# Performance work log

Measured on AMD Instinct MI355X. Metric: run time of the kernel, lower is better.

## Reference

```python
import jax, jax.numpy as jnp
import numpy as np

N_NODES = 100000
N_EDGES = 1600000
IN_CH, HID_CH, OUT_CH = 128, 128, 64


def glorot(key, fan_in, fan_out):
    lim = np.sqrt(6.0 / (fan_in + fan_out)).astype(np.float32)
    return jax.random.uniform(key, (fan_in, fan_out), jnp.float32, -lim, lim)


def gcn_conv(x, src, dst, W, b):
    """PyG GCNConv: add self-loops, symmetric deg^-1/2 normalization,
    linear transform, scatter-add aggregation at targets, plus bias."""
    n = x.shape[0]
    xw = x @ W  # [N, F_out]
    loop = jnp.arange(n)
    s = jnp.concatenate([src, loop])  # sources (message origin)
    d = jnp.concatenate([dst, loop])  # targets (aggregation site)
    deg = jax.ops.segment_sum(jnp.ones_like(d, dtype=xw.dtype), d, num_segments=n)
    dinv = jnp.where(deg > 0, jax.lax.rsqrt(deg), 0.0)
    norm = dinv[s] * dinv[d]  # [E+N]
    out = jax.ops.segment_sum(norm[:, None] * xw[s], d, num_segments=n)
    return out + b


def setup_inputs() -> dict:
    key = jax.random.key(0)
    ks = jax.random.split(key, 8)
    x = jax.random.normal(ks[0], (N_NODES, IN_CH), jnp.float32)
    edge_index = jax.random.randint(ks[1], (2, N_EDGES), 0, N_NODES, jnp.int64)
    return {
        "x": x,
        "edge_index": edge_index,
        "W1": glorot(ks[2], IN_CH, HID_CH),
        "b1": jnp.zeros((HID_CH,), jnp.float32),
        "W2": glorot(ks[3], HID_CH, HID_CH),
        "b2": jnp.zeros((HID_CH,), jnp.float32),
        "W3": glorot(ks[4], HID_CH, OUT_CH),
        "b3": jnp.zeros((OUT_CH,), jnp.float32),
    }


def reference(x, edge_index, W1, b1, W2, b2, W3, b3):
    src, dst = edge_index[0], edge_index[1]
    # eval mode: dropout is identity
    h = jax.nn.relu(gcn_conv(x, src, dst, W1, b1))
    h = jax.nn.relu(gcn_conv(h, src, dst, W2, b2))
    h = gcn_conv(h, src, dst, W3, b3)
    return jax.nn.log_softmax(h, axis=1)
```

## Files before the change

kernel.cpp:

```cpp
#include <hip/hip_runtime.h>
#include <math.h>


#define NN 100000
#define NE 1600000
#define NBUK 391
#define BCAP 4608

typedef float floatx4 __attribute__((ext_vector_type(4)));
typedef short short8 __attribute__((ext_vector_type(8)));

__device__ __forceinline__ unsigned short f2bf(float f) {
    unsigned u = __float_as_uint(f);
    unsigned r = (u + 0x7fffu + ((u >> 16) & 1u)) >> 16;
    return (unsigned short)r;
}
__device__ __forceinline__ float bflo(unsigned u) { return __uint_as_float(u << 16); }
__device__ __forceinline__ float bfhi(unsigned u) { return __uint_as_float(u & 0xffff0000u); }

__global__ __launch_bounds__(256) void k_wprep(const float* __restrict__ W, unsigned short* __restrict__ Wtg,
                                               int K, int NC) {
    int idx = blockIdx.x * 256 + threadIdx.x;
    if (idx >= NC * K) return;
    int n = idx / K, k = idx - n * K;
    Wtg[idx] = f2bf(W[k * NC + n]);
}

__global__ __launch_bounds__(256) void k_bucket(const int4* __restrict__ src4, const int4* __restrict__ dst4,
                                                int* __restrict__ bcur, int* __restrict__ bbuf, int E) {
    __shared__ int hist[NBUK];
    __shared__ int base[NBUK];
    int t = threadIdx.x;
    for (int b = t; b < NBUK; b += 256) hist[b] = 0;
    __syncthreads();
    int E4 = E >> 2;
    int q0 = blockIdx.x * 1024;
    #pragma unroll
    for (int j = 0; j < 4; j++) {
        int q = q0 + j * 256 + t;
        if (q < E4) {
            int4 d = dst4[q];
            atomicAdd(&hist[d.x >> 8], 1);
            atomicAdd(&hist[d.y >> 8], 1);
            atomicAdd(&hist[d.z >> 8], 1);
            atomicAdd(&hist[d.w >> 8], 1);
        }
    }
    __syncthreads();
    for (int b = t; b < NBUK; b += 256) {
        int c = hist[b];
        base[b] = c ? atomicAdd(&bcur[b], c) : 0;
        hist[b] = 0;
    }
    __syncthreads();
    #pragma unroll
    for (int j = 0; j < 4; j++) {
        int q = q0 + j * 256 + t;
        if (q < E4) {
            int4 s = src4[q];
            int4 d = dst4[q];
            int sv[4] = {s.x, s.y, s.z, s.w};
            int dv[4] = {d.x, d.y, d.z, d.w};
            #pragma unroll
            for (int u = 0; u < 4; u++) {
                int b = dv[u] >> 8;
                int r = atomicAdd(&hist[b], 1);
                int pos = base[b] + r;
                if (pos < BCAP) bbuf[b * BCAP + pos] = (sv[u] << 8) | (dv[u] & 255);
            }
        }
    }
}

__global__ void k_scanbuckets(const int* __restrict__ bcur, int* __restrict__ bbase, int nb,
                              int* __restrict__ row_ptr, int n, int E) {
    int lane = threadIdx.x;
    int carry = 0;
    for (int base = 0; base < nb; base += 64) {
        int idx = base + lane;
        int v = (idx < nb) ? min(bcur[idx], BCAP) : 0;
        int orig = v;
        #pragma unroll
        for (int o = 1; o < 64; o <<= 1) {
            int u = __shfl_up(v, o);
            if (lane >= o) v += u;
        }
        if (idx < nb) bbase[idx] = carry + v - orig;
        carry += __shfl(v, 63);
    }
    if (lane == 0) row_ptr[n] = E;
}

__global__ __launch_bounds__(256) void k_build(const int* __restrict__ bcur, const int* __restrict__ bbase,
                                               const int* __restrict__ bbuf,
                                               int* __restrict__ row_ptr, int* __restrict__ csr, int N) {
    __shared__ int sh[256];
    __shared__ int cur[256];
    __shared__ int loc[BCAP];
    int b = blockIdx.x, t = threadIdx.x;
    int cnt = min(bcur[b], BCAP);
    int gbase = bbase[b];
    const int* bp = bbuf + b * BCAP;
    sh[t] = 0;
    __syncthreads();
    for (int i = t; i < cnt; i += 256) atomicAdd(&sh[bp[i] & 255], 1);
    __syncthreads();
    int v = sh[t];
    for (int o = 1; o < 256; o <<= 1) {
        int u = (t >= o) ? sh[t - o] : 0;
        __syncthreads();
        sh[t] += u;
        __syncthreads();
    }
    int excl = sh[t] - v;
    int node = b * 256 + t;
    if (node < N) row_ptr[node] = gbase + excl;
    cur[t] = excl;
    __syncthreads();
    for (int i = t; i < cnt; i += 256) {
        int p = bp[i];
        int r = atomicAdd(&cur[p & 255], 1);
        loc[r] = p >> 8;
    }
    __syncthreads();
    for (int i = t; i < cnt; i += 256) csr[gbase + i] = loc[i];
}

__global__ __launch_bounds__(256) void k_dinv(const int* __restrict__ row_ptr, float* __restrict__ dinv, int n) {
    int i = blockIdx.x * 256 + threadIdx.x;
    if (i < n) {
        int d = row_ptr[i + 1] - row_ptr[i];
        dinv[i] = rsqrtf((float)d + 1.0f);
    }
}


template <int NC, bool CVT>
__global__ __launch_bounds__(256) void k_mfma(const void* __restrict__ Av, const unsigned short* __restrict__ Wtg,
                                              const float* __restrict__ dinv, unsigned short* __restrict__ Y, int M) {
    constexpr int K = 128;
    constexpr int NT = NC / 16;
    __shared__ unsigned short Wt[NC][136];
    int t = threadIdx.x;
    constexpr int NV = NC * K / 8;
    for (int idx = t; idx < NV; idx += 256) {
        int nrow = idx >> 4;
        int chunk = idx & 15;
        *(uint4*)&Wt[nrow][chunk * 8] = *(const uint4*)(Wtg + nrow * K + chunk * 8);
    }
    __syncthreads();
    int lane = t & 63, wid = t >> 6;
    int col = lane & 15, quad = lane >> 4;
    int nstrips = M / 16;
    int s = blockIdx.x * 4 + wid;
    if (s >= nstrips) return;
    int row0 = s * 16;

    short8 af[4];
    if (CVT) {
        const float* Af = (const float*)Av + (size_t)(row0 + col) * K + quad * 8;
        #pragma unroll
        for (int ks = 0; ks < 4; ks++) {
            float4 f0 = *(const float4*)(Af + ks * 32);
            float4 f1 = *(const float4*)(Af + ks * 32 + 4);
            short8 v;
            v[0] = (short)f2bf(f0.x); v[1] = (short)f2bf(f0.y); v[2] = (short)f2bf(f0.z); v[3] = (short)f2bf(f0.w);
            v[4] = (short)f2bf(f1.x); v[5] = (short)f2bf(f1.y); v[6] = (short)f2bf(f1.z); v[7] = (short)f2bf(f1.w);
            af[ks] = v;
        }
    } else {
        const unsigned short* Ab = (const unsigned short*)Av + (size_t)(row0 + col) * K + quad * 8;
        #pragma unroll
        for (int ks = 0; ks < 4; ks++) af[ks] = *(const short8*)(Ab + ks * 32);
    }

    floatx4 acc[NT];
    #pragma unroll
    for (int i = 0; i < NT; i++) acc[i] = (floatx4){0.f, 0.f, 0.f, 0.f};
    #pragma unroll
    for (int ks = 0; ks < 4; ks++) {
        #pragma unroll
        for (int nt = 0; nt < NT; nt++) {
            short8 bfrag = *(const short8*)&Wt[nt * 16 + col][ks * 32 + quad * 8];
            acc[nt] = __builtin_amdgcn_mfma_f32_16x16x32_bf16(af[ks], bfrag, acc[nt], 0, 0, 0);
        }
    }
    #pragma unroll
    for (int r = 0; r < 4; r++) {
        int row = row0 + quad * 4 + r;
        float dv = dinv[row];
        #pragma unroll
        for (int nt = 0; nt < NT; nt++) {
            Y[(size_t)row * NC + nt * 16 + col] = f2bf(acc[nt][r] * dv);
        }
    }
}


__device__ __forceinline__ void acc8(float* a, uint4 v) {
    a[0] += bflo(v.x); a[1] += bfhi(v.x);
    a[2] += bflo(v.y); a[3] += bfhi(v.y);
    a[4] += bflo(v.z); a[5] += bfhi(v.z);
    a[6] += bflo(v.w); a[7] += bfhi(v.w);
}

__global__ __launch_bounds__(256) void k_gather_relu_bf(const uint4* __restrict__ y, const int* __restrict__ csr,
                                                        const int* __restrict__ row_ptr, const float* __restrict__ dinv,
                                                        const float* __restrict__ bias, uint4* __restrict__ h, int n) {
    int node = blockIdx.x * 16 + (threadIdx.x >> 4);
    int c = threadIdx.x & 15;
    if (node >= n) return;
    int s0 = row_ptr[node], s1 = row_ptr[node + 1];
    float a[8] = {};
    acc8(a, y[(size_t)node * 16 + c]);
    int p = s0;
    int i0, i1, i2, i3, i4, i5, i6, i7;
    if (p + 8 <= s1) {
        i0 = csr[p]; i1 = csr[p+1]; i2 = csr[p+2]; i3 = csr[p+3];
        i4 = csr[p+4]; i5 = csr[p+5]; i6 = csr[p+6]; i7 = csr[p+7];
        while (true) {
            uint4 v0 = y[(size_t)i0 * 16 + c], v1 = y[(size_t)i1 * 16 + c];
            uint4 v2 = y[(size_t)i2 * 16 + c], v3 = y[(size_t)i3 * 16 + c];
            uint4 v4 = y[(size_t)i4 * 16 + c], v5 = y[(size_t)i5 * 16 + c];
            uint4 v6 = y[(size_t)i6 * 16 + c], v7 = y[(size_t)i7 * 16 + c];
            p += 8;
            bool nxt = (p + 8 <= s1);
            if (nxt) {
                i0 = csr[p]; i1 = csr[p+1]; i2 = csr[p+2]; i3 = csr[p+3];
                i4 = csr[p+4]; i5 = csr[p+5]; i6 = csr[p+6]; i7 = csr[p+7];
            }
            acc8(a, v0); acc8(a, v1); acc8(a, v2); acc8(a, v3);
            acc8(a, v4); acc8(a, v5); acc8(a, v6); acc8(a, v7);
            if (!nxt) break;
        }
    }
    if (p + 4 <= s1) {
        int j0 = csr[p], j1 = csr[p+1], j2 = csr[p+2], j3 = csr[p+3];
        uint4 v0 = y[(size_t)j0 * 16 + c], v1 = y[(size_t)j1 * 16 + c];
        uint4 v2 = y[(size_t)j2 * 16 + c], v3 = y[(size_t)j3 * 16 + c];
        acc8(a, v0); acc8(a, v1); acc8(a, v2); acc8(a, v3);
        p += 4;
    }
    for (; p < s1; p++) acc8(a, y[(size_t)csr[p] * 16 + c]);
    float s = dinv[node];
    float4 b0 = ((const float4*)bias)[c * 2];
    float4 b1 = ((const float4*)bias)[c * 2 + 1];
    float r0 = fmaxf(s * a[0] + b0.x, 0.f), r1 = fmaxf(s * a[1] + b0.y, 0.f);
    float r2 = fmaxf(s * a[2] + b0.z, 0.f), r3 = fmaxf(s * a[3] + b0.w, 0.f);
    float r4 = fmaxf(s * a[4] + b1.x, 0.f), r5 = fmaxf(s * a[5] + b1.y, 0.f);
    float r6 = fmaxf(s * a[6] + b1.z, 0.f), r7 = fmaxf(s * a[7] + b1.w, 0.f);
    uint4 o;
    o.x = ((unsigned)f2bf(r1) << 16) | f2bf(r0);
    o.y = ((unsigned)f2bf(r3) << 16) | f2bf(r2);
    o.z = ((unsigned)f2bf(r5) << 16) | f2bf(r4);
    o.w = ((unsigned)f2bf(r7) << 16) | f2bf(r6);
    h[(size_t)node * 16 + c] = o;
}

__global__ __launch_bounds__(256) void k_gather_lsm_bf(const uint4* __restrict__ y, const int* __restrict__ csr,
                                                       const int* __restrict__ row_ptr, const float* __restrict__ dinv,
                                                       const float* __restrict__ bias, float4* __restrict__ out4, int n) {
    int node = blockIdx.x * 32 + (threadIdx.x >> 3);
    int c = threadIdx.x & 7;
    if (node >= n) return;
    int s0 = row_ptr[node], s1 = row_ptr[node + 1];
    float a[8] = {};
    acc8(a, y[(size_t)node * 8 + c]);
    int p = s0;
    int i0, i1, i2, i3, i4, i5, i6, i7;
    if (p + 8 <= s1) {
        i0 = csr[p]; i1 = csr[p+1]; i2 = csr[p+2]; i3 = csr[p+3];
        i4 = csr[p+4]; i5 = csr[p+5]; i6 = csr[p+6]; i7 = csr[p+7];
        while (true) {
            uint4 v0 = y[(size_t)i0 * 8 + c], v1 = y[(size_t)i1 * 8 + c];
            uint4 v2 = y[(size_t)i2 * 8 + c], v3 = y[(size_t)i3 * 8 + c];
            uint4 v4 = y[(size_t)i4 * 8 + c], v5 = y[(size_t)i5 * 8 + c];
            uint4 v6 = y[(size_t)i6 * 8 + c], v7 = y[(size_t)i7 * 8 + c];
            p += 8;
            bool nxt = (p + 8 <= s1);
            if (nxt) {
                i0 = csr[p]; i1 = csr[p+1]; i2 = csr[p+2]; i3 = csr[p+3];
                i4 = csr[p+4]; i5 = csr[p+5]; i6 = csr[p+6]; i7 = csr[p+7];
            }
            acc8(a, v0); acc8(a, v1); acc8(a, v2); acc8(a, v3);
            acc8(a, v4); acc8(a, v5); acc8(a, v6); acc8(a, v7);
            if (!nxt) break;
        }
    }
    if (p + 4 <= s1) {
        int j0 = csr[p], j1 = csr[p+1], j2 = csr[p+2], j3 = csr[p+3];
        uint4 v0 = y[(size_t)j0 * 8 + c], v1 = y[(size_t)j1 * 8 + c];
        uint4 v2 = y[(size_t)j2 * 8 + c], v3 = y[(size_t)j3 * 8 + c];
        acc8(a, v0); acc8(a, v1); acc8(a, v2); acc8(a, v3);
        p += 4;
    }
    for (; p < s1; p++) acc8(a, y[(size_t)csr[p] * 8 + c]);
    float s = dinv[node];
    float4 b0 = ((const float4*)bias)[c * 2];
    float4 b1 = ((const float4*)bias)[c * 2 + 1];
    float v[8];
    v[0] = s * a[0] + b0.x; v[1] = s * a[1] + b0.y; v[2] = s * a[2] + b0.z; v[3] = s * a[3] + b0.w;
    v[4] = s * a[4] + b1.x; v[5] = s * a[5] + b1.y; v[6] = s * a[6] + b1.z; v[7] = s * a[7] + b1.w;
    float m = v[0];
    #pragma unroll
    for (int i = 1; i < 8; i++) m = fmaxf(m, v[i]);
    #pragma unroll
    for (int o = 4; o > 0; o >>= 1) m = fmaxf(m, __shfl_xor(m, o));
    float sum = 0.f;
    #pragma unroll
    for (int i = 0; i < 8; i++) sum += expf(v[i] - m);
    #pragma unroll
    for (int o = 4; o > 0; o >>= 1) sum += __shfl_xor(sum, o);
    float lse = m + logf(sum);
    out4[(size_t)node * 16 + c * 2]     = make_float4(v[0] - lse, v[1] - lse, v[2] - lse, v[3] - lse);
    out4[(size_t)node * 16 + c * 2 + 1] = make_float4(v[4] - lse, v[5] - lse, v[6] - lse, v[7] - lse);
}


extern "C" void kernel_launch(void* const* d_in, const int* in_sizes, int n_in,
                              void* d_out, int out_size, void* d_ws, size_t ws_size,
                              hipStream_t stream) {
    const float* x  = (const float*)d_in[0];
    const int*   ei = (const int*)d_in[1];
    const float* W1 = (const float*)d_in[2];
    const float* b1 = (const float*)d_in[3];
    const float* W2 = (const float*)d_in[4];
    const float* b2 = (const float*)d_in[5];
    const float* W3 = (const float*)d_in[6];
    const float* b3 = (const float*)d_in[7];
    float* out = (float*)d_out;

    const int N = NN, E = NE;
    const int nb = (N + 255) / 256;

    char* ws = (char*)d_ws;
    size_t off = 0;
    auto alloc = [&](size_t bytes) -> void* {
        void* p = ws + off;
        off += bytes;
        off = (off + 255) & ~(size_t)255;
        return p;
    };
    int*            row_ptr = (int*)alloc((size_t)(N + 1) * 4);
    float*          dinvv   = (float*)alloc((size_t)N * 4);
    int*            bcur    = (int*)alloc(512 * 4);
    int*            bbase   = (int*)alloc(512 * 4);
    int*            bbuf    = (int*)alloc((size_t)NBUK * BCAP * 4);
    int*            csr     = (int*)alloc((size_t)E * 4);
    unsigned short* wt1     = (unsigned short*)alloc(128 * 128 * 2);
    unsigned short* wt2     = (unsigned short*)alloc(128 * 128 * 2);
    unsigned short* wt3     = (unsigned short*)alloc(64 * 128 * 2);
    unsigned short* yb      = (unsigned short*)alloc((size_t)N * 128 * 2);
    unsigned short* hb      = (unsigned short*)alloc((size_t)N * 128 * 2);
    (void)ws_size; (void)in_sizes; (void)n_in; (void)out_size;

    const int* srcp = ei;
    const int* dstp = ei + E;

    hipMemsetAsync(bcur, 0, 512 * 4, stream);
    k_wprep<<<64, 256, 0, stream>>>(W1, wt1, 128, 128);
    k_wprep<<<64, 256, 0, stream>>>(W2, wt2, 128, 128);
    k_wprep<<<32, 256, 0, stream>>>(W3, wt3, 128, 64);
    k_bucket<<<(E + 4095) / 4096, 256, 0, stream>>>((const int4*)srcp, (const int4*)dstp, bcur, bbuf, E);
    k_scanbuckets<<<1, 64, 0, stream>>>(bcur, bbase, NBUK, row_ptr, N, E);
    k_build<<<NBUK, 256, 0, stream>>>(bcur, bbase, bbuf, row_ptr, csr, N);
    k_dinv<<<nb, 256, 0, stream>>>(row_ptr, dinvv, N);

    const int nstrips = N / 16;
    const int gmm = (nstrips + 3) / 4;
    k_mfma<128, true><<<gmm, 256, 0, stream>>>(x, wt1, dinvv, yb, N);
    k_gather_relu_bf<<<N / 16, 256, 0, stream>>>((const uint4*)yb, csr, row_ptr, dinvv, b1, (uint4*)hb, N);
    k_mfma<128, false><<<gmm, 256, 0, stream>>>(hb, wt2, dinvv, yb, N);
    k_gather_relu_bf<<<N / 16, 256, 0, stream>>>((const uint4*)yb, csr, row_ptr, dinvv, b2, (uint4*)hb, N);
    k_mfma<64, false><<<gmm, 256, 0, stream>>>(hb, wt3, dinvv, yb, N);
    k_gather_lsm_bf<<<N / 32, 256, 0, stream>>>((const uint4*)yb, csr, row_ptr, dinvv, b3, (float4*)out, N);
}
```

Baseline: 342.3 us.

## Sort CSR neighbor lists per node and simplify gather loops to 4-way unroll

Adds a per-node insertion sort of the source indices inside the CSR build kernel, so each node's neighbors are read in ascending address order during the gathers, which may improve cache locality. The two gather kernels also drop their 8-way software-pipelined index prefetch in favour of a plain 4-way unrolled loop. The sort adds serial per-thread work to the CSR build, and the simpler loop keeps fewer loads in flight, which may hurt latency hiding.

After: 378.3 us. 1.11x slower.

```diff
diff --git a/kernel.cpp b/kernel.cpp
--- a/kernel.cpp
+++ b/kernel.cpp
@@ -123,6 +123,20 @@
         loc[r] = p >> 8;
     }
     __syncthreads();
+    {
+        int seg0 = excl;
+        int seg1 = cur[t];
+        for (int i = seg0 + 1; i < seg1; i++) {
+            int val = loc[i];
+            int j = i - 1;
+            while (j >= seg0 && loc[j] > val) {
+                loc[j + 1] = loc[j];
+                j--;
+            }
+            loc[j + 1] = val;
+        }
+    }
+    __syncthreads();
     for (int i = t; i < cnt; i += 256) csr[gbase + i] = loc[i];
 }
 
@@ -214,32 +228,13 @@
     float a[8] = {};
     acc8(a, y[(size_t)node * 16 + c]);
     int p = s0;
-    int i0, i1, i2, i3, i4, i5, i6, i7;
-    if (p + 8 <= s1) {
-        i0 = csr[p]; i1 = csr[p+1]; i2 = csr[p+2]; i3 = csr[p+3];
-        i4 = csr[p+4]; i5 = csr[p+5]; i6 = csr[p+6]; i7 = csr[p+7];
-        while (true) {
-            uint4 v0 = y[(size_t)i0 * 16 + c], v1 = y[(size_t)i1 * 16 + c];
-            uint4 v2 = y[(size_t)i2 * 16 + c], v3 = y[(size_t)i3 * 16 + c];
-            uint4 v4 = y[(size_t)i4 * 16 + c], v5 = y[(size_t)i5 * 16 + c];
-            uint4 v6 = y[(size_t)i6 * 16 + c], v7 = y[(size_t)i7 * 16 + c];
-            p += 8;
-            bool nxt = (p + 8 <= s1);
-            if (nxt) {
-                i0 = csr[p]; i1 = csr[p+1]; i2 = csr[p+2]; i3 = csr[p+3];
-                i4 = csr[p+4]; i5 = csr[p+5]; i6 = csr[p+6]; i7 = csr[p+7];
-            }
-            acc8(a, v0); acc8(a, v1); acc8(a, v2); acc8(a, v3);
-            acc8(a, v4); acc8(a, v5); acc8(a, v6); acc8(a, v7);
-            if (!nxt) break;
-        }
-    }
-    if (p + 4 <= s1) {
-        int j0 = csr[p], j1 = csr[p+1], j2 = csr[p+2], j3 = csr[p+3];
-        uint4 v0 = y[(size_t)j0 * 16 + c], v1 = y[(size_t)j1 * 16 + c];
-        uint4 v2 = y[(size_t)j2 * 16 + c], v3 = y[(size_t)j3 * 16 + c];
+    for (; p + 4 <= s1; p += 4) {
+        int i0 = csr[p], i1 = csr[p + 1], i2 = csr[p + 2], i3 = csr[p + 3];
+        uint4 v0 = y[(size_t)i0 * 16 + c];
+        uint4 v1 = y[(size_t)i1 * 16 + c];
+        uint4 v2 = y[(size_t)i2 * 16 + c];
+        uint4 v3 = y[(size_t)i3 * 16 + c];
         acc8(a, v0); acc8(a, v1); acc8(a, v2); acc8(a, v3);
-        p += 4;
     }
     for (; p < s1; p++) acc8(a, y[(size_t)csr[p] * 16 + c]);
     float s = dinv[node];
@@ -267,32 +262,13 @@
     float a[8] = {};
     acc8(a, y[(size_t)node * 8 + c]);
     int p = s0;
-    int i0, i1, i2, i3, i4, i5, i6, i7;
-    if (p + 8 <= s1) {
-        i0 = csr[p]; i1 = csr[p+1]; i2 = csr[p+2]; i3 = csr[p+3];
-        i4 = csr[p+4]; i5 = csr[p+5]; i6 = csr[p+6]; i7 = csr[p+7];
-        while (true) {
-            uint4 v0 = y[(size_t)i0 * 8 + c], v1 = y[(size_t)i1 * 8 + c];
-            uint4 v2 = y[(size_t)i2 * 8 + c], v3 = y[(size_t)i3 * 8 + c];
-            uint4 v4 = y[(size_t)i4 * 8 + c], v5 = y[(size_t)i5 * 8 + c];
-            uint4 v6 = y[(size_t)i6 * 8 + c], v7 = y[(size_t)i7 * 8 + c];
-            p += 8;
-            bool nxt = (p + 8 <= s1);
-            if (nxt) {
-                i0 = csr[p]; i1 = csr[p+1]; i2 = csr[p+2]; i3 = csr[p+3];
-                i4 = csr[p+4]; i5 = csr[p+5]; i6 = csr[p+6]; i7 = csr[p+7];
-            }
-            acc8(a, v0); acc8(a, v1); acc8(a, v2); acc8(a, v3);
-            acc8(a, v4); acc8(a, v5); acc8(a, v6); acc8(a, v7);
-            if (!nxt) break;
-        }
-    }
-    if (p + 4 <= s1) {
-        int j0 = csr[p], j1 = csr[p+1], j2 = csr[p+2], j3 = csr[p+3];
-        uint4 v0 = y[(size_t)j0 * 8 + c], v1 = y[(size_t)j1 * 8 + c];
-        uint4 v2 = y[(size_t)j2 * 8 + c], v3 = y[(size_t)j3 * 8 + c];
+    for (; p + 4 <= s1; p += 4) {
+        int i0 = csr[p], i1 = csr[p + 1], i2 = csr[p + 2], i3 = csr[p + 3];
+        uint4 v0 = y[(size_t)i0 * 8 + c];
+        uint4 v1 = y[(size_t)i1 * 8 + c];
+        uint4 v2 = y[(size_t)i2 * 8 + c];
+        uint4 v3 = y[(size_t)i3 * 8 + c];
         acc8(a, v0); acc8(a, v1); acc8(a, v2); acc8(a, v3);
-        p += 4;
     }
     for (; p < s1; p++) acc8(a, y[(size_t)csr[p] * 8 + c]);
     float s = dinv[node];
```
